# Kernel optimization log

Measured on AMD Instinct MI355X. Metric: run time of the kernel, lower is better.

The kernel has to match this reference:

```python
import jax, jax.numpy as jnp
import numpy as np

B, S, D, H = 2, 2048, 1024, 16
HD = D // H  # 64


def setup_inputs() -> dict:
    key = jax.random.key(0)
    ks = jax.random.split(key, 12)
    scale = 1.0 / np.sqrt(D)
    inp = {
        "input_query": jax.random.normal(ks[0], (B, S, D), jnp.float32),
        "input_key": jax.random.normal(ks[1], (B, S, D), jnp.float32),
        "input_value": jax.random.normal(ks[2], (B, S, D), jnp.float32),
        "mask": jax.random.randint(ks[3], (B, 1, S), 0, 2, jnp.int32),
        # torch nn.Linear params: y = x @ W.T + b, W shape (out, in)
        "wq": jax.random.uniform(ks[4], (D, D), jnp.float32, -scale, scale),
        "bq": jax.random.uniform(ks[5], (D,), jnp.float32, -scale, scale),
        "wk": jax.random.uniform(ks[6], (D, D), jnp.float32, -scale, scale),
        "bk": jax.random.uniform(ks[7], (D,), jnp.float32, -scale, scale),
        "wv": jax.random.uniform(ks[8], (D, D), jnp.float32, -scale, scale),
        "bv": jax.random.uniform(ks[9], (D,), jnp.float32, -scale, scale),
        "wo": jax.random.uniform(ks[10], (D, D), jnp.float32, -scale, scale),
        "bo": jax.random.uniform(ks[11], (D,), jnp.float32, -scale, scale),
    }
    return inp


def _split_heads(x):
    # (B, S, D) -> (B, H, S, HD)
    return x.reshape(B, S, H, HD).transpose(0, 2, 1, 3)


def reference(input_query, input_key, input_value, mask, wq, bq, wk, bk, wv, bv, wo, bo):
    q = _split_heads(input_query @ wq.T + bq)
    k = _split_heads(input_key @ wk.T + bk)
    v = _split_heads(input_value @ wv.T + bv)

    # scaled dot-product attention (materializes [B,H,S,S] as the original does)
    scores = jnp.einsum("bhqd,bhkd->bhqk", q, k) / np.sqrt(HD).astype(np.float32)
    # mask: (B, 1, S) -> unsqueeze(1) -> (B, 1, 1, S); fill -1e9 where mask == 0
    m = mask[:, None, :, :]
    scores = jnp.where(m == 0, jnp.float32(-1e9), scores)
    p_attn = jax.nn.softmax(scores, axis=-1)  # dropout is identity (rate 0 / eval)

    out = jnp.einsum("bhqk,bhkd->bhqd", p_attn, v)
    out = out.transpose(0, 2, 1, 3).reshape(B, S, D)
    return out @ wo.T + bo
```

## Files before the change

kernel.cpp:

```cpp
#include <hip/hip_runtime.h>
#include <math.h>

#define BB 2
#define SS 2048
#define DD 1024
#define HH 16
#define HD 64

typedef short short8 __attribute__((ext_vector_type(8)));
typedef float floatx4 __attribute__((ext_vector_type(4)));
typedef float floatx16 __attribute__((ext_vector_type(16)));
typedef unsigned int uintx2 __attribute__((ext_vector_type(2)));

__device__ inline ushort f2bf_rne(float x) {
    union { float f; unsigned u; } v; v.f = x;
    unsigned r = v.u + 0x7FFFu + ((v.u >> 16) & 1u);
    return (ushort)(r >> 16);
}
__device__ inline float bf2f(ushort h) {
    union { unsigned u; float f; } v; v.u = ((unsigned)h) << 16;
    return v.f;
}
__device__ inline unsigned cvt_pk_bf16(float lo, float hi) {
    unsigned r;
    asm("v_cvt_pk_bf16_f32 %0, %1, %2" : "=v"(r) : "v"(lo), "v"(hi));
    return r;
}
__device__ inline short8 mk_pf(uintx2 x, uintx2 y) {
    union { unsigned u[4]; short8 s; } t;
    t.u[0] = x[0]; t.u[1] = y[0]; t.u[2] = x[1]; t.u[3] = y[1];
    return t.s;
}

__global__ __launch_bounds__(256)
void convert_bf16(const float* __restrict__ xq, const float* __restrict__ xk,
                  const float* __restrict__ xv,
                  const float* __restrict__ wq, const float* __restrict__ wk,
                  const float* __restrict__ wv, const float* __restrict__ wo,
                  ushort* __restrict__ Xq, ushort* __restrict__ Xk,
                  ushort* __restrict__ Xv,
                  ushort* __restrict__ Wq, ushort* __restrict__ Wk,
                  ushort* __restrict__ Wv, ushort* __restrict__ Wo)
{
    const int z = blockIdx.z;
    const size_t i = ((size_t)blockIdx.x * 256 + threadIdx.x) * 8;

    const float* src;
    ushort* dst;
    size_t off;
    if (z < 3) {
        src = (z == 0) ? xq : (z == 1) ? xk : xv;
        dst = (z == 0) ? Xq : (z == 1) ? Xk : Xv;
        off = i;
    } else {
        const int seg = (int)(i >> 20);
        off = i & ((1u << 20) - 1);
        src = (seg == 0) ? wq : (seg == 1) ? wk : (seg == 2) ? wv : wo;
        dst = (seg == 0) ? Wq : (seg == 1) ? Wk : (seg == 2) ? Wv : Wo;
    }
    float x[8];
    *(float4*)&x[0] = *(const float4*)(src + off);
    *(float4*)&x[4] = *(const float4*)(src + off + 4);
    short8 h8;
#pragma unroll
    for (int j = 0; j < 8; ++j) h8[j] = (short)f2bf_rne(x[j]);
    *(short8*)&dst[off] = h8;
}

#define LDK 40

__global__ __launch_bounds__(256, 3)
void qkv_gemm(const ushort* __restrict__ Xq, const ushort* __restrict__ Xk,
              const ushort* __restrict__ Xv,
              const ushort* __restrict__ Wq, const ushort* __restrict__ Wk,
              const ushort* __restrict__ Wv,
              const float* __restrict__ bq, const float* __restrict__ bk,
              const float* __restrict__ bv, const int* __restrict__ mask,
              ushort* __restrict__ Qo, ushort* __restrict__ Ko,
              ushort* __restrict__ Vo, float qscale)
{
    __shared__ ushort Alds[128][LDK];
    __shared__ ushort Blds[128][LDK];

    const int z   = blockIdx.z;
    const int tid = threadIdx.x;

    const ushort* X    = (z == 0) ? Xq : (z == 1) ? Xk : Xv;
    const ushort* W    = (z == 0) ? Wq : (z == 1) ? Wk : Wv;
    const float*  bias = (z == 0) ? bq : (z == 1) ? bk : bv;
    const float   osc  = (z == 0) ? qscale : 1.0f;

    const int lane = tid & 63;
    const int wave = tid >> 6;
    const int wr = wave >> 1;
    const int wc = wave & 1;
    const int lt = lane & 15;
    const int lq = lane >> 4;
    const int m0 = blockIdx.y * 128;
    const int n0 = blockIdx.x * 128;

    floatx4 acc[4][4];
#pragma unroll
    for (int mi = 0; mi < 4; ++mi)
#pragma unroll
        for (int ni = 0; ni < 4; ++ni) acc[mi][ni] = (floatx4)0.0f;

    const int srow = tid >> 1;
    const int sks  = (tid & 1) << 4;
    const size_t xrow = (size_t)(m0 + srow) * DD;
    const size_t wrow = (size_t)(n0 + srow) * DD;

    for (int k0 = 0; k0 < DD; k0 += 32) {
        const short8 a0 = *(const short8*)(X + xrow + k0 + sks);
        const short8 a1 = *(const short8*)(X + xrow + k0 + sks + 8);
        const short8 b0 = *(const short8*)(W + wrow + k0 + sks);
        const short8 b1 = *(const short8*)(W + wrow + k0 + sks + 8);

        __syncthreads();
        *(short8*)&Alds[srow][sks]     = a0;
        *(short8*)&Alds[srow][sks + 8] = a1;
        *(short8*)&Blds[srow][sks]     = b0;
        *(short8*)&Blds[srow][sks + 8] = b1;
        __syncthreads();

        short8 af[4], bf_[4];
#pragma unroll
        for (int mi = 0; mi < 4; ++mi)
            af[mi] = *(const short8*)&Alds[wr * 64 + mi * 16 + lt][lq * 8];
#pragma unroll
        for (int ni = 0; ni < 4; ++ni)
            bf_[ni] = *(const short8*)&Blds[wc * 64 + ni * 16 + lt][lq * 8];

#pragma unroll
        for (int mi = 0; mi < 4; ++mi)
#pragma unroll
            for (int ni = 0; ni < 4; ++ni)
                acc[mi][ni] = __builtin_amdgcn_mfma_f32_16x16x32_bf16(af[mi], bf_[ni], acc[mi][ni], 0, 0, 0);
    }

    float bbv[4];
#pragma unroll
    for (int ni = 0; ni < 4; ++ni) bbv[ni] = bias[n0 + wc * 64 + ni * 16 + lt];

    if (z == 2) {
#pragma unroll
        for (int mi = 0; mi < 4; ++mi) {
            const int mb  = m0 + wr * 64 + mi * 16 + lq * 4;
            const int bb_ = mb >> 11;
            const int s   = mb & (SS - 1);
            const int4 mm = *(const int4*)(mask + bb_ * SS + s);
            const float mf0 = (float)mm.x, mf1 = (float)mm.y;
            const float mf2 = (float)mm.z, mf3 = (float)mm.w;
#pragma unroll
            for (int ni = 0; ni < 4; ++ni) {
                const int n = n0 + wc * 64 + ni * 16 + lt;
                const int h = n >> 6;
                ushort4 pack;
                pack.x = f2bf_rne((acc[mi][ni][0] + bbv[ni]) * mf0);
                pack.y = f2bf_rne((acc[mi][ni][1] + bbv[ni]) * mf1);
                pack.z = f2bf_rne((acc[mi][ni][2] + bbv[ni]) * mf2);
                pack.w = f2bf_rne((acc[mi][ni][3] + bbv[ni]) * mf3);
                *(ushort4*)&Vo[(size_t)((bb_ * HH + h) * HD + (n & 63)) * SS + s] = pack;
            }
        }
    } else {
        ushort* C = z ? Ko : Qo;
#pragma unroll
        for (int mi = 0; mi < 4; ++mi) {
            const int mb  = m0 + wr * 64 + mi * 16 + lq * 4;
            const int bb_ = mb >> 11;
            const int s   = mb & (SS - 1);
            float mf[4] = {1.0f, 1.0f, 1.0f, 1.0f};
            if (z == 1) {
                const int4 mm = *(const int4*)(mask + bb_ * SS + s);
                mf[0] = (float)mm.x; mf[1] = (float)mm.y;
                mf[2] = (float)mm.z; mf[3] = (float)mm.w;
            }
#pragma unroll
            for (int ni = 0; ni < 4; ++ni) {
                const int n = n0 + wc * 64 + ni * 16 + lt;
                const int h = n >> 6;
#pragma unroll
                for (int r = 0; r < 4; ++r) {
                    C[(size_t)((bb_ * HH + h) * SS + (s + r)) * HD + (n & 63)] =
                        f2bf_rne((acc[mi][ni][r] + bbv[ni]) * osc * mf[r]);
                }
            }
        }
    }
}

#define ATQ 128
#define LDV 68

__global__ __launch_bounds__(256, 2)
void attn_mfma(const ushort* __restrict__ Qb, const ushort* __restrict__ Kb,
               const ushort* __restrict__ Vt, const int* __restrict__ mask,
               ushort* __restrict__ Ob)
{
    __shared__ __align__(16) ushort Klds[2][64][LDV];
    __shared__ __align__(16) ushort Vlds[2][64][LDV];
    __shared__ float CmbO[2][2][16][64];
    __shared__ float CmbL[2][16][64];
    __shared__ int   Wsum[4];

    const int tid  = threadIdx.x;
    const int lane = tid & 63;
    const int wave = tid >> 6;
    const int ll   = lane & 31;
    const int hi   = lane >> 5;
    const int qh   = wave & 1;
    const int ks   = wave >> 1;

    const int bid    = blockIdx.x;
    const int xcd    = bid & 7;
    const int slot   = bid >> 3;
    const int bhloc  = slot >> 4;
    const int qi     = slot & 15;
    const int bh     = xcd * 4 + bhloc;
    const int b      = bh >> 4;
    const int q0     = qi * ATQ;

    const size_t sbase = (size_t)bh * SS * HD;
    const size_t vbase = (size_t)bh * HD * SS;

    {
        const int4 ma = *(const int4*)(mask + b * SS + tid * 8);
        const int4 mb = *(const int4*)(mask + b * SS + tid * 8 + 4);
        int s = ma.x + ma.y + ma.z + ma.w + mb.x + mb.y + mb.z + mb.w;
#pragma unroll
        for (int w = 32; w >= 1; w >>= 1) s += __shfl_xor(s, w);
        if (lane == 0) Wsum[wave] = s;
    }

    short8 ones;
#pragma unroll
    for (int j = 0; j < 8; ++j) ones[j] = (short)0x3F80;

    short8 qf[2][4];
#pragma unroll
    for (int g = 0; g < 2; ++g) {
        const size_t qrow = sbase + (size_t)(q0 + qh * 64 + g * 32 + ll) * HD;
#pragma unroll
        for (int dc = 0; dc < 4; ++dc)
            qf[g][dc] = *(const short8*)(Qb + qrow + dc * 16 + hi * 8);
    }

    floatx16 oacc[2][2];
    floatx16 lacc[2];
#pragma unroll
    for (int g = 0; g < 2; ++g) {
        oacc[g][0] = (floatx16)0.0f;
        oacc[g][1] = (floatx16)0.0f;
        lacc[g]    = (floatx16)0.0f;
    }

    const int srow = tid >> 2;
    const int sp8  = (tid & 3) << 4;

    short8 kr0, kr1, vr0, vr1;

    {
        const size_t koff = sbase + (size_t)srow * HD + sp8;
        kr0 = *(const short8*)(Kb + koff);
        kr1 = *(const short8*)(Kb + koff + 8);
        const size_t voff = vbase + (size_t)srow * SS + sp8;
        vr0 = *(const short8*)(Vt + voff);
        vr1 = *(const short8*)(Vt + voff + 8);
        *(short8*)&Klds[0][srow][sp8]     = kr0;
        *(short8*)&Klds[0][srow][sp8 + 8] = kr1;
        *(short8*)&Vlds[0][srow][sp8]     = vr0;
        *(short8*)&Vlds[0][srow][sp8 + 8] = vr1;
    }

    const int NT = SS / 64;
    for (int kt = 0; kt < NT; ++kt) {
        const int cur = kt & 1;
        __syncthreads();

        if (kt + 1 < NT) {
            const int k0n = (kt + 1) * 64;
            const size_t koff = sbase + (size_t)(k0n + srow) * HD + sp8;
            kr0 = *(const short8*)(Kb + koff);
            kr1 = *(const short8*)(Kb + koff + 8);
            const size_t voff = vbase + (size_t)srow * SS + k0n + sp8;
            vr0 = *(const short8*)(Vt + voff);
            vr1 = *(const short8*)(Vt + voff + 8);
        }

        short8 kf[4];
#pragma unroll
        for (int dc = 0; dc < 4; ++dc)
            kf[dc] = *(const short8*)&Klds[cur][ks * 32 + ll][dc * 16 + hi * 8];

        short8 pf[2][2];
#pragma unroll
        for (int g = 0; g < 2; ++g) {
            floatx16 sacc = (floatx16)0.0f;
#pragma unroll
            for (int dc = 0; dc < 4; ++dc)
                sacc = __builtin_amdgcn_mfma_f32_32x32x16_bf16(kf[dc], qf[g][dc], sacc, 0, 0, 0);

            float p[16];
#pragma unroll
            for (int r = 0; r < 16; ++r) p[r] = exp2f(sacc[r]);

            const unsigned pk_a = cvt_pk_bf16(p[0],  p[1]);
            const unsigned pk_b = cvt_pk_bf16(p[2],  p[3]);
            const unsigned pk_c = cvt_pk_bf16(p[4],  p[5]);
            const unsigned pk_d = cvt_pk_bf16(p[6],  p[7]);
            const unsigned pk_e = cvt_pk_bf16(p[8],  p[9]);
            const unsigned pk_f = cvt_pk_bf16(p[10], p[11]);
            const unsigned pk_g = cvt_pk_bf16(p[12], p[13]);
            const unsigned pk_h = cvt_pk_bf16(p[14], p[15]);
            const uintx2 s1 = __builtin_amdgcn_permlane32_swap(pk_a, pk_c, false, false);
            const uintx2 s2 = __builtin_amdgcn_permlane32_swap(pk_b, pk_d, false, false);
            const uintx2 s3 = __builtin_amdgcn_permlane32_swap(pk_e, pk_g, false, false);
            const uintx2 s4 = __builtin_amdgcn_permlane32_swap(pk_f, pk_h, false, false);
            pf[g][0] = mk_pf(s1, s2);
            pf[g][1] = mk_pf(s3, s4);
        }

#pragma unroll
        for (int g = 0; g < 2; ++g) {
            lacc[g] = __builtin_amdgcn_mfma_f32_32x32x16_bf16(pf[g][0], ones, lacc[g], 0, 0, 0);
            lacc[g] = __builtin_amdgcn_mfma_f32_32x32x16_bf16(pf[g][1], ones, lacc[g], 0, 0, 0);
        }

#pragma unroll
        for (int dn = 0; dn < 2; ++dn) {
            const short8 vf0 = *(const short8*)&Vlds[cur][dn * 32 + ll][ks * 32 + hi * 8];
            const short8 vf1 = *(const short8*)&Vlds[cur][dn * 32 + ll][ks * 32 + 16 + hi * 8];
#pragma unroll
            for (int g = 0; g < 2; ++g) {
                oacc[g][dn] = __builtin_amdgcn_mfma_f32_32x32x16_bf16(pf[g][0], vf0, oacc[g][dn], 0, 0, 0);
                oacc[g][dn] = __builtin_amdgcn_mfma_f32_32x32x16_bf16(pf[g][1], vf1, oacc[g][dn], 0, 0, 0);
            }
        }

        if (kt + 1 < NT) {
            const int nxt = cur ^ 1;
            *(short8*)&Klds[nxt][srow][sp8]     = kr0;
            *(short8*)&Klds[nxt][srow][sp8 + 8] = kr1;
            *(short8*)&Vlds[nxt][srow][sp8]     = vr0;
            *(short8*)&Vlds[nxt][srow][sp8 + 8] = vr1;
        }
    }

#pragma unroll
    for (int g = 0; g < 2; ++g) {
        __syncthreads();
        if (wave >= 2) {
#pragma unroll
            for (int dn = 0; dn < 2; ++dn)
#pragma unroll
                for (int r = 0; r < 16; ++r)
                    CmbO[wave - 2][dn][r][lane] = oacc[g][dn][r];
#pragma unroll
            for (int r = 0; r < 16; ++r)
                CmbL[wave - 2][r][lane] = lacc[g][r];
        }
        __syncthreads();
        if (wave < 2) {
#pragma unroll
            for (int dn = 0; dn < 2; ++dn)
#pragma unroll
                for (int r = 0; r < 16; ++r)
                    oacc[g][dn][r] += CmbO[wave][dn][r][lane];
#pragma unroll
            for (int r = 0; r < 16; ++r)
                lacc[g][r] += CmbL[wave][r][lane];
        }
    }

    if (wave < 2) {
        const int h = bh & 15;
        const float nmf = (float)(SS - (Wsum[0] + Wsum[1] + Wsum[2] + Wsum[3]));
#pragma unroll
        for (int g = 0; g < 2; ++g) {
            float linv[16];
#pragma unroll
            for (int r = 0; r < 16; ++r) linv[r] = 1.0f / (lacc[g][r] - nmf);
#pragma unroll
            for (int dn = 0; dn < 2; ++dn)
#pragma unroll
                for (int r = 0; r < 16; ++r) {
                    const int q = q0 + qh * 64 + g * 32 + (r & 3) + 8 * (r >> 2) + 4 * hi;
                    Ob[(size_t)(b * SS + q) * DD + h * HD + dn * 32 + ll] =
                        f2bf_rne(oacc[g][dn][r] * linv[r]);
                }
        }
    }
}

__global__ __launch_bounds__(256, 3)
void o_gemm(const ushort* __restrict__ A, const ushort* __restrict__ B,
            const float* __restrict__ bias, float* __restrict__ out)
{
    __shared__ ushort sA[128][LDK];
    __shared__ ushort sB[64][LDK];

    const int tid  = threadIdx.x;
    const int lane = tid & 63;
    const int wave = tid >> 6;
    const int wr = wave >> 1;
    const int wc = wave & 1;
    const int lt = lane & 15;
    const int lq = lane >> 4;
    const int m0 = blockIdx.y * 128;
    const int n0 = blockIdx.x * 64;

    floatx4 acc[4][2];
#pragma unroll
    for (int mi = 0; mi < 4; ++mi)
#pragma unroll
        for (int ni = 0; ni < 2; ++ni) acc[mi][ni] = (floatx4)0.0f;

    const int arow = tid >> 1, apart = (tid & 1) << 4;
    const int brow = tid >> 2, bpart = (tid & 3) << 3;

    for (int k0 = 0; k0 < DD; k0 += 32) {
        const size_t aoff = (size_t)(m0 + arow) * DD + k0 + apart;
        const size_t boff = (size_t)(n0 + brow) * DD + k0 + bpart;
        const short8 a0 = *(const short8*)(A + aoff);
        const short8 a1 = *(const short8*)(A + aoff + 8);
        const short8 b0 = *(const short8*)(B + boff);

        __syncthreads();
        *(short8*)&sA[arow][apart]     = a0;
        *(short8*)&sA[arow][apart + 8] = a1;
        *(short8*)&sB[brow][bpart]     = b0;
        __syncthreads();

        short8 af[4], bf_[2];
#pragma unroll
        for (int mi = 0; mi < 4; ++mi)
            af[mi] = *(const short8*)&sA[wr * 64 + mi * 16 + lt][lq * 8];
#pragma unroll
        for (int ni = 0; ni < 2; ++ni)
            bf_[ni] = *(const short8*)&sB[wc * 32 + ni * 16 + lt][lq * 8];

#pragma unroll
        for (int mi = 0; mi < 4; ++mi)
#pragma unroll
            for (int ni = 0; ni < 2; ++ni)
                acc[mi][ni] = __builtin_amdgcn_mfma_f32_16x16x32_bf16(af[mi], bf_[ni], acc[mi][ni], 0, 0, 0);
    }

#pragma unroll
    for (int mi = 0; mi < 4; ++mi)
#pragma unroll
        for (int ni = 0; ni < 2; ++ni) {
            const int n = n0 + wc * 32 + ni * 16 + lt;
            const float bb = bias[n];
#pragma unroll
            for (int r = 0; r < 4; ++r) {
                const int m = m0 + wr * 64 + mi * 16 + lq * 4 + r;
                out[(size_t)m * DD + n] = acc[mi][ni][r] + bb;
            }
        }
}

extern "C" void kernel_launch(void* const* d_in, const int* in_sizes, int n_in,
                              void* d_out, int out_size, void* d_ws, size_t ws_size,
                              hipStream_t stream) {
    const float* xq   = (const float*)d_in[0];
    const float* xk   = (const float*)d_in[1];
    const float* xv   = (const float*)d_in[2];
    const int*   mask = (const int*)d_in[3];
    const float* wq   = (const float*)d_in[4];
    const float* bq   = (const float*)d_in[5];
    const float* wk   = (const float*)d_in[6];
    const float* bk   = (const float*)d_in[7];
    const float* wv   = (const float*)d_in[8];
    const float* bv   = (const float*)d_in[9];
    const float* wo   = (const float*)d_in[10];
    const float* bo   = (const float*)d_in[11];
    float* out = (float*)d_out;

    const size_t n = (size_t)BB * SS * DD;
    const size_t w1 = (size_t)DD * DD;

    ushort* Xqb = (ushort*)d_ws;
    ushort* Xkb = Xqb + n;
    ushort* Xvb = Xkb + n;
    ushort* Kb  = Xvb + n;
    ushort* Vt  = Kb + n;
    ushort* Wob = Vt + n;
    ushort* Ob  = Xqb;

    ushort* Qb  = (ushort*)out;
    ushort* Wqb = Qb + n;
    ushort* Wkb = Wqb + w1;
    ushort* Wvb = Wkb + w1;

    const float qscale = 0.125f * 1.44269504088896340736f;

    dim3 gc(2048, 1, 4);
    convert_bf16<<<gc, 256, 0, stream>>>(xq, xk, xv, wq, wk, wv, wo,
                                         Xqb, Xkb, Xvb, Wqb, Wkb, Wvb, Wob);

    dim3 g1(DD / 128, (BB * SS) / 128, 3);
    qkv_gemm<<<g1, 256, 0, stream>>>(Xqb, Xkb, Xvb, Wqb, Wkb, Wvb,
                                     bq, bk, bv, mask, Qb, Kb, Vt, qscale);

    attn_mfma<<<dim3(512), 256, 0, stream>>>(Qb, Kb, Vt, mask, Ob);

    dim3 g2(DD / 64, (BB * SS) / 128);
    o_gemm<<<g2, 256, 0, stream>>>(Ob, Wob, bo, out);
}
```

Measured before the change: 241.0 us.

## Split attention across eight waves per block and widen output GEMM tile

The attention kernel moves from 256 to 512 threads, so each wave handles one 32-row query group instead of two. This halves per-wave register state, which should allow more waves in flight. The cross-wave reduction buffer now reuses the K/V shared memory, and exp2f is replaced by the hardware exp2 intrinsic. The output projection GEMM tile grows from 128x64 to 128x128, which halves the grid and gives each A-tile more reuse, at the cost of more registers and fewer blocks.

```diff
diff --git a/kernel.cpp b/kernel.cpp
--- a/kernel.cpp
+++ b/kernel.cpp
@@ -16,10 +16,6 @@
     union { float f; unsigned u; } v; v.f = x;
     unsigned r = v.u + 0x7FFFu + ((v.u >> 16) & 1u);
     return (ushort)(r >> 16);
-}
-__device__ inline float bf2f(ushort h) {
-    union { unsigned u; float f; } v; v.u = ((unsigned)h) << 16;
-    return v.f;
 }
 __device__ inline unsigned cvt_pk_bf16(float lo, float hi) {
     unsigned r;
@@ -190,27 +186,23 @@
     }
 }
 
-#define ATQ 128
 #define LDV 68
 
-__global__ __launch_bounds__(256, 2)
+__global__ __launch_bounds__(512, 4)
 void attn_mfma(const ushort* __restrict__ Qb, const ushort* __restrict__ Kb,
                const ushort* __restrict__ Vt, const int* __restrict__ mask,
                ushort* __restrict__ Ob)
 {
-    __shared__ __align__(16) ushort Klds[2][64][LDV];
-    __shared__ __align__(16) ushort Vlds[2][64][LDV];
-    __shared__ float CmbO[2][2][16][64];
-    __shared__ float CmbL[2][16][64];
-    __shared__ int   Wsum[4];
+    __shared__ __align__(16) ushort KVlds[4][64][LDV];
+    __shared__ int Wsum[8];
 
     const int tid  = threadIdx.x;
     const int lane = tid & 63;
     const int wave = tid >> 6;
     const int ll   = lane & 31;
     const int hi   = lane >> 5;
-    const int qh   = wave & 1;
-    const int ks   = wave >> 1;
+    const int qh   = wave & 3;
+    const int ks   = wave >> 2;
 
     const int bid    = blockIdx.x;
     const int xcd    = bid & 7;
@@ -219,15 +211,14 @@
     const int qi     = slot & 15;
     const int bh     = xcd * 4 + bhloc;
     const int b      = bh >> 4;
-    const int q0     = qi * ATQ;
+    const int q0     = qi * 128;
 
     const size_t sbase = (size_t)bh * SS * HD;
     const size_t vbase = (size_t)bh * HD * SS;
 
     {
-        const int4 ma = *(const int4*)(mask + b * SS + tid * 8);
-        const int4 mb = *(const int4*)(mask + b * SS + tid * 8 + 4);
-        int s = ma.x + ma.y + ma.z + ma.w + mb.x + mb.y + mb.z + mb.w;
+        const int4 ma = *(const int4*)(mask + b * SS + tid * 4);
+        int s = ma.x + ma.y + ma.z + ma.w;
 #pragma unroll
         for (int w = 32; w >= 1; w >>= 1) s += __shfl_xor(s, w);
         if (lane == 0) Wsum[wave] = s;
@@ -237,40 +228,29 @@
 #pragma unroll
     for (int j = 0; j < 8; ++j) ones[j] = (short)0x3F80;
 
-    short8 qf[2][4];
-#pragma unroll
-    for (int g = 0; g < 2; ++g) {
-        const size_t qrow = sbase + (size_t)(q0 + qh * 64 + g * 32 + ll) * HD;
+    short8 qf[4];
+    {
+        const size_t qrow = sbase + (size_t)(q0 + qh * 32 + ll) * HD;
 #pragma unroll
         for (int dc = 0; dc < 4; ++dc)
-            qf[g][dc] = *(const short8*)(Qb + qrow + dc * 16 + hi * 8);
-    }
-
-    floatx16 oacc[2][2];
-    floatx16 lacc[2];
-#pragma unroll
-    for (int g = 0; g < 2; ++g) {
-        oacc[g][0] = (floatx16)0.0f;
-        oacc[g][1] = (floatx16)0.0f;
-        lacc[g]    = (floatx16)0.0f;
-    }
-
-    const int srow = tid >> 2;
-    const int sp8  = (tid & 3) << 4;
-
-    short8 kr0, kr1, vr0, vr1;
+            qf[dc] = *(const short8*)(Qb + qrow + dc * 16 + hi * 8);
+    }
+
+    floatx16 oacc[2];
+    oacc[0] = (floatx16)0.0f;
+    oacc[1] = (floatx16)0.0f;
+    floatx16 lacc = (floatx16)0.0f;
+
+    const int srow = tid >> 3;
+    const int sp8  = (tid & 7) << 3;
+
+    short8 kr, vr;
 
     {
-        const size_t koff = sbase + (size_t)srow * HD + sp8;
-        kr0 = *(const short8*)(Kb + koff);
-        kr1 = *(const short8*)(Kb + koff + 8);
-        const size_t voff = vbase + (size_t)srow * SS + sp8;
-        vr0 = *(const short8*)(Vt + voff);
-        vr1 = *(const short8*)(Vt + voff + 8);
-        *(short8*)&Klds[0][srow][sp8]     = kr0;
-        *(short8*)&Klds[0][srow][sp8 + 8] = kr1;
-        *(short8*)&Vlds[0][srow][sp8]     = vr0;
-        *(short8*)&Vlds[0][srow][sp8 + 8] = vr1;
+        kr = *(const short8*)(Kb + sbase + (size_t)srow * HD + sp8);
+        vr = *(const short8*)(Vt + vbase + (size_t)srow * SS + sp8);
+        *(short8*)&KVlds[0][srow][sp8] = kr;
+        *(short8*)&KVlds[2][srow][sp8] = vr;
     }
 
     const int NT = SS / 64;
@@ -280,116 +260,101 @@
 
         if (kt + 1 < NT) {
             const int k0n = (kt + 1) * 64;
-            const size_t koff = sbase + (size_t)(k0n + srow) * HD + sp8;
-            kr0 = *(const short8*)(Kb + koff);
-            kr1 = *(const short8*)(Kb + koff + 8);
-            const size_t voff = vbase + (size_t)srow * SS + k0n + sp8;
-            vr0 = *(const short8*)(Vt + voff);
-            vr1 = *(const short8*)(Vt + voff + 8);
+            kr = *(const short8*)(Kb + sbase + (size_t)(k0n + srow) * HD + sp8);
+            vr = *(const short8*)(Vt + vbase + (size_t)srow * SS + k0n + sp8);
         }
 
         short8 kf[4];
 #pragma unroll
         for (int dc = 0; dc < 4; ++dc)
-            kf[dc] = *(const short8*)&Klds[cur][ks * 32 + ll][dc * 16 + hi * 8];
-
-        short8 pf[2][2];
-#pragma unroll
-        for (int g = 0; g < 2; ++g) {
-            floatx16 sacc = (floatx16)0.0f;
-#pragma unroll
-            for (int dc = 0; dc < 4; ++dc)
-                sacc = __builtin_amdgcn_mfma_f32_32x32x16_bf16(kf[dc], qf[g][dc], sacc, 0, 0, 0);
-
-            float p[16];
-#pragma unroll
-            for (int r = 0; r < 16; ++r) p[r] = exp2f(sacc[r]);
-
-            const unsigned pk_a = cvt_pk_bf16(p[0],  p[1]);
-            const unsigned pk_b = cvt_pk_bf16(p[2],  p[3]);
-            const unsigned pk_c = cvt_pk_bf16(p[4],  p[5]);
-            const unsigned pk_d = cvt_pk_bf16(p[6],  p[7]);
-            const unsigned pk_e = cvt_pk_bf16(p[8],  p[9]);
-            const unsigned pk_f = cvt_pk_bf16(p[10], p[11]);
-            const unsigned pk_g = cvt_pk_bf16(p[12], p[13]);
-            const unsigned pk_h = cvt_pk_bf16(p[14], p[15]);
-            const uintx2 s1 = __builtin_amdgcn_permlane32_swap(pk_a, pk_c, false, false);
-            const uintx2 s2 = __builtin_amdgcn_permlane32_swap(pk_b, pk_d, false, false);
-            const uintx2 s3 = __builtin_amdgcn_permlane32_swap(pk_e, pk_g, false, false);
-            const uintx2 s4 = __builtin_amdgcn_permlane32_swap(pk_f, pk_h, false, false);
-            pf[g][0] = mk_pf(s1, s2);
-            pf[g][1] = mk_pf(s3, s4);
-        }
-
-#pragma unroll
-        for (int g = 0; g < 2; ++g) {
-            lacc[g] = __builtin_amdgcn_mfma_f32_32x32x16_bf16(pf[g][0], ones, lacc[g], 0, 0, 0);
-            lacc[g] = __builtin_amdgcn_mfma_f32_32x32x16_bf16(pf[g][1], ones, lacc[g], 0, 0, 0);
-        }
+            kf[dc] = *(const short8*)&KVlds[cur][ks * 32 + ll][dc * 16 + hi * 8];
+
+        floatx16 sacc = (floatx16)0.0f;
+#pragma unroll
+        for (int dc = 0; dc < 4; ++dc)
+            sacc = __builtin_amdgcn_mfma_f32_32x32x16_bf16(kf[dc], qf[dc], sacc, 0, 0, 0);
+
+        float p[16];
+#pragma unroll
+        for (int r = 0; r < 16; ++r) p[r] = __builtin_amdgcn_exp2f(sacc[r]);
+
+        const unsigned pk_a = cvt_pk_bf16(p[0],  p[1]);
+        const unsigned pk_b = cvt_pk_bf16(p[2],  p[3]);
+        const unsigned pk_c = cvt_pk_bf16(p[4],  p[5]);
+        const unsigned pk_d = cvt_pk_bf16(p[6],  p[7]);
+        const unsigned pk_e = cvt_pk_bf16(p[8],  p[9]);
+        const unsigned pk_f = cvt_pk_bf16(p[10], p[11]);
+        const unsigned pk_g = cvt_pk_bf16(p[12], p[13]);
+        const unsigned pk_h = cvt_pk_bf16(p[14], p[15]);
+        const uintx2 s1 = __builtin_amdgcn_permlane32_swap(pk_a, pk_c, false, false);
+        const uintx2 s2 = __builtin_amdgcn_permlane32_swap(pk_b, pk_d, false, false);
+        const uintx2 s3 = __builtin_amdgcn_permlane32_swap(pk_e, pk_g, false, false);
+        const uintx2 s4 = __builtin_amdgcn_permlane32_swap(pk_f, pk_h, false, false);
+        const short8 pf0 = mk_pf(s1, s2);
+        const short8 pf1 = mk_pf(s3, s4);
+
+        lacc = __builtin_amdgcn_mfma_f32_32x32x16_bf16(pf0, ones, lacc, 0, 0, 0);
+        lacc = __builtin_amdgcn_mfma_f32_32x32x16_bf16(pf1, ones, lacc, 0, 0, 0);
 
 #pragma unroll
         for (int dn = 0; dn < 2; ++dn) {
-            const short8 vf0 = *(const short8*)&Vlds[cur][dn * 32 + ll][ks * 32 + hi * 8];
-            const short8 vf1 = *(const short8*)&Vlds[cur][dn * 32 + ll][ks * 32 + 16 + hi * 8];
-#pragma unroll
-            for (int g = 0; g < 2; ++g) {
-                oacc[g][dn] = __builtin_amdgcn_mfma_f32_32x32x16_bf16(pf[g][0], vf0, oacc[g][dn], 0, 0, 0);
-                oacc[g][dn] = __builtin_amdgcn_mfma_f32_32x32x16_bf16(pf[g][1], vf1, oacc[g][dn], 0, 0, 0);
-            }
+            const short8 vf0 = *(const short8*)&KVlds[2 + cur][dn * 32 + ll][ks * 32 + hi * 8];
+            const short8 vf1 = *(const short8*)&KVlds[2 + cur][dn * 32 + ll][ks * 32 + 16 + hi * 8];
+            oacc[dn] = __builtin_amdgcn_mfma_f32_32x32x16_bf16(pf0, vf0, oacc[dn], 0, 0, 0);
+            oacc[dn] = __builtin_amdgcn_mfma_f32_32x32x16_bf16(pf1, vf1, oacc[dn], 0, 0, 0);
         }
 
         if (kt + 1 < NT) {
             const int nxt = cur ^ 1;
-            *(short8*)&Klds[nxt][srow][sp8]     = kr0;
-            *(short8*)&Klds[nxt][srow][sp8 + 8] = kr1;
-            *(short8*)&Vlds[nxt][srow][sp8]     = vr0;
-            *(short8*)&Vlds[nxt][srow][sp8 + 8] = vr1;
-        }
-    }
-
-#pragma unroll
-    for (int g = 0; g < 2; ++g) {
-        __syncthreads();
-        if (wave >= 2) {
+            *(short8*)&KVlds[nxt][srow][sp8]     = kr;
+            *(short8*)&KVlds[2 + nxt][srow][sp8] = vr;
+        }
+    }
+
+    float* Cmb = (float*)&KVlds[0][0][0];
+#pragma unroll
+    for (int ph = 0; ph < 2; ++ph) {
+        __syncthreads();
+        if (ks == 1 && (qh >> 1) == ph) {
+            const int sl = qh & 1;
 #pragma unroll
             for (int dn = 0; dn < 2; ++dn)
 #pragma unroll
                 for (int r = 0; r < 16; ++r)
-                    CmbO[wave - 2][dn][r][lane] = oacc[g][dn][r];
+                    Cmb[((sl * 2 + dn) * 16 + r) * 64 + lane] = oacc[dn][r];
 #pragma unroll
             for (int r = 0; r < 16; ++r)
-                CmbL[wave - 2][r][lane] = lacc[g][r];
-        }
-        __syncthreads();
-        if (wave < 2) {
+                Cmb[4096 + (sl * 16 + r) * 64 + lane] = lacc[r];
+        }
+        __syncthreads();
+        if (ks == 0 && (qh >> 1) == ph) {
+            const int sl = qh & 1;
 #pragma unroll
             for (int dn = 0; dn < 2; ++dn)
 #pragma unroll
                 for (int r = 0; r < 16; ++r)
-                    oacc[g][dn][r] += CmbO[wave][dn][r][lane];
+                    oacc[dn][r] += Cmb[((sl * 2 + dn) * 16 + r) * 64 + lane];
 #pragma unroll
             for (int r = 0; r < 16; ++r)
-                lacc[g][r] += CmbL[wave][r][lane];
-        }
-    }
-
-    if (wave < 2) {
+                lacc[r] += Cmb[4096 + (sl * 16 + r) * 64 + lane];
+        }
+    }
+
+    if (ks == 0) {
         const int h = bh & 15;
-        const float nmf = (float)(SS - (Wsum[0] + Wsum[1] + Wsum[2] + Wsum[3]));
-#pragma unroll
-        for (int g = 0; g < 2; ++g) {
-            float linv[16];
-#pragma unroll
-            for (int r = 0; r < 16; ++r) linv[r] = 1.0f / (lacc[g][r] - nmf);
-#pragma unroll
-            for (int dn = 0; dn < 2; ++dn)
-#pragma unroll
-                for (int r = 0; r < 16; ++r) {
-                    const int q = q0 + qh * 64 + g * 32 + (r & 3) + 8 * (r >> 2) + 4 * hi;
-                    Ob[(size_t)(b * SS + q) * DD + h * HD + dn * 32 + ll] =
-                        f2bf_rne(oacc[g][dn][r] * linv[r]);
-                }
-        }
+        const float nmf = (float)(SS - (Wsum[0] + Wsum[1] + Wsum[2] + Wsum[3]
+                                      + Wsum[4] + Wsum[5] + Wsum[6] + Wsum[7]));
+        float linv[16];
+#pragma unroll
+        for (int r = 0; r < 16; ++r) linv[r] = 1.0f / (lacc[r] - nmf);
+#pragma unroll
+        for (int dn = 0; dn < 2; ++dn)
+#pragma unroll
+            for (int r = 0; r < 16; ++r) {
+                const int q = q0 + qh * 32 + (r & 3) + 8 * (r >> 2) + 4 * hi;
+                Ob[(size_t)(b * SS + q) * DD + h * HD + dn * 32 + ll] =
+                    f2bf_rne(oacc[dn][r] * linv[r]);
+            }
     }
 }
 
@@ -398,7 +363,7 @@
             const float* __restrict__ bias, float* __restrict__ out)
 {
     __shared__ ushort sA[128][LDK];
-    __shared__ ushort sB[64][LDK];
+    __shared__ ushort sB[128][LDK];
 
     const int tid  = threadIdx.x;
     const int lane = tid & 63;
@@ -408,50 +373,52 @@
     const int lt = lane & 15;
     const int lq = lane >> 4;
     const int m0 = blockIdx.y * 128;
-    const int n0 = blockIdx.x * 64;
-
-    floatx4 acc[4][2];
+    const int n0 = blockIdx.x * 128;
+
+    floatx4 acc[4][4];
 #pragma unroll
     for (int mi = 0; mi < 4; ++mi)
 #pragma unroll
-        for (int ni = 0; ni < 2; ++ni) acc[mi][ni] = (floatx4)0.0f;
-
-    const int arow = tid >> 1, apart = (tid & 1) << 4;
-    const int brow = tid >> 2, bpart = (tid & 3) << 3;
+        for (int ni = 0; ni < 4; ++ni) acc[mi][ni] = (floatx4)0.0f;
+
+    const int srow = tid >> 1;
+    const int sks  = (tid & 1) << 4;
+    const size_t arow_ = (size_t)(m0 + srow) * DD;
+    const size_t brow_ = (size_t)(n0 + srow) * DD;
 
     for (int k0 = 0; k0 < DD; k0 += 32) {
-        const size_t aoff = (size_t)(m0 + arow) * DD + k0 + apart;
-        const size_t boff = (size_t)(n0 + brow) * DD + k0 + bpart;
-        const short8 a0 = *(const short8*)(A + aoff);
-        const short8 a1 = *(const short8*)(A + aoff + 8);
-        const short8 b0 = *(const short8*)(B + boff);
-
-        __syncthreads();
-        *(short8*)&sA[arow][apart]     = a0;
-        *(short8*)&sA[arow][apart + 8] = a1;
-        *(short8*)&sB[brow][bpart]     = b0;
-        __syncthreads();
-
-        short8 af[4], bf_[2];
+        const short8 a0 = *(const short8*)(A + arow_ + k0 + sks);
+        const short8 a1 = *(const short8*)(A + arow_ + k0 + sks + 8);
+        const short8 b0 = *(const short8*)(B + brow_ + k0 + sks);
+        const short8 b1 = *(const short8*)(B + brow_ + k0 + sks + 8);
+
+        __syncthreads();
+        *(short8*)&sA[srow][sks]     = a0;
+        *(short8*)&sA[srow][sks + 8] = a1;
+        *(short8*)&sB[srow][sks]     = b0;
+        *(short8*)&sB[srow][sks + 8] = b1;
+        __syncthreads();
+
+        short8 af[4], bf_[4];
 #pragma unroll
         for (int mi = 0; mi < 4; ++mi)
             af[mi] = *(const short8*)&sA[wr * 64 + mi * 16 + lt][lq * 8];
 #pragma unroll
-        for (int ni = 0; ni < 2; ++ni)
-            bf_[ni] = *(const short8*)&sB[wc * 32 + ni * 16 + lt][lq * 8];
+        for (int ni = 0; ni < 4; ++ni)
+            bf_[ni] = *(const short8*)&sB[wc * 64 + ni * 16 + lt][lq * 8];
 
 #pragma unroll
         for (int mi = 0; mi < 4; ++mi)
 #pragma unroll
-            for (int ni = 0; ni < 2; ++ni)
+            for (int ni = 0; ni < 4; ++ni)
                 acc[mi][ni] = __builtin_amdgcn_mfma_f32_16x16x32_bf16(af[mi], bf_[ni], acc[mi][ni], 0, 0, 0);
     }
 
 #pragma unroll
     for (int mi = 0; mi < 4; ++mi)
 #pragma unroll
-        for (int ni = 0; ni < 2; ++ni) {
-            const int n = n0 + wc * 32 + ni * 16 + lt;
+        for (int ni = 0; ni < 4; ++ni) {
+            const int n = n0 + wc * 64 + ni * 16 + lt;
             const float bb = bias[n];
 #pragma unroll
             for (int r = 0; r < 4; ++r) {
@@ -504,8 +471,8 @@
     qkv_gemm<<<g1, 256, 0, stream>>>(Xqb, Xkb, Xvb, Wqb, Wkb, Wvb,
                                      bq, bk, bv, mask, Qb, Kb, Vt, qscale);
 
-    attn_mfma<<<dim3(512), 256, 0, stream>>>(Qb, Kb, Vt, mask, Ob);
-
-    dim3 g2(DD / 64, (BB * SS) / 128);
+    attn_mfma<<<dim3(512), 512, 0, stream>>>(Qb, Kb, Vt, mask, Ob);
+
+    dim3 g2(DD / 128, (BB * SS) / 128);
     o_gemm<<<g2, 256, 0, stream>>>(Ob, Wob, bo, out);
 }
```

New measurement: 226.7 us. 5.9% less time.
